# Optimization experiments

Hardware: AMD Instinct MI355X
Metric: run time of the kernel (lower is better)

The kernel has to match this reference:

```python
import jax, jax.numpy as jnp
import numpy as np


def setup_inputs() -> dict:
    key = jax.random.key(0)
    k1, k2 = jax.random.split(key)
    B, T, D, E = 4, 4096, 2048, 64
    x = jax.random.normal(k1, (B, T, D), dtype=jnp.float32)
    # nn.Linear default init ~ U(-1/sqrt(D), 1/sqrt(D)); scaled normal is fine for a numeric baseline
    W = jax.random.normal(k2, (D, E), dtype=jnp.float32) * (1.0 / np.sqrt(D))
    b = jnp.zeros((E,), dtype=jnp.float32)
    return {"x": x, "W": W, "b": b}


TOPK = 2


def reference(x, W, b):
    # logits: (B, T, E)
    logits = jnp.einsum("btd,de->bte", x, W) + b
    probs = jax.nn.softmax(logits, axis=-1)
    topk_vals, topk_idx = jax.lax.top_k(probs, TOPK)
    return topk_idx, topk_vals
```

## Files before the change

### kernel.cpp

```cpp
#include <hip/hip_runtime.h>
#include <math.h>


#define D_DIM 2048
#define E_DIM 64
#define M_DIM 16384
#define RM 32
#define BKC 64
#define NCHW 8
#define XSTR 68

typedef _Float16 half8 __attribute__((ext_vector_type(8)));
typedef float floatx4 __attribute__((ext_vector_type(4)));
typedef unsigned int uint;

__global__ __launch_bounds__(256) void split_w_kernel(
    const float* __restrict__ Wm, _Float16* __restrict__ wsT)
{
    const int tid = threadIdx.x;
    const int n   = tid & 63;
    const int kk0 = tid >> 6;
    const int g   = blockIdx.x;
    #pragma unroll
    for (int r = 0; r < 8; r++) {
        const int kk = kk0 + r * 4;
        const float v = Wm[(size_t)(g * 32 + kk) * E_DIM + n];
        const _Float16 h = (_Float16)v;
        const _Float16 l = (_Float16)((v - (float)h) * 2048.0f);
        const int t = n >> 4, cc = n & 15, qd = kk >> 3, j = kk & 7;
        const size_t base = (size_t)((g * 4 + t) * 2) * 512 + (size_t)(qd * 16 + cc) * 8 + j;
        wsT[base]       = h;
        wsT[base + 512] = l;
    }
}

__global__ __launch_bounds__(256, 2) void router_mfma_kernel(
    const float* __restrict__ x, const _Float16* __restrict__ wsT,
    const float* __restrict__ bias, float* __restrict__ out)
{
    __shared__ uint xbuf[4][2][RM * XSTR];

    const int lane = threadIdx.x & 63;
    const int wave = threadIdx.x >> 6;
    const int c    = lane & 15;
    const int quad = lane >> 4;
    const int c8   = lane & 7;
    const int rq   = lane >> 3;
    const int r0   = blockIdx.x * RM;
    const int kb   = wave * (D_DIM / 4);

    const float* xg = x + (size_t)(r0 + rq) * D_DIM + kb + c8 * 8;
    const _Float16* wbase = wsT + (size_t)(wave * 16) * 4096 + lane * 8;

    floatx4 accm[2][4] = {};
    floatx4 accl[2][4] = {};
    float4 xa[8], xb[8];
    half8 wh0[4], wl0[4], wh1[4], wl1[4];

    auto loadx = [&](int n, float4* dst) {
        const int nn = n < NCHW ? n : NCHW - 1;
        #pragma unroll
        for (int i = 0; i < 4; i++) {
            const float* p = xg + (size_t)i * 8 * D_DIM + nn * BKC;
            dst[2 * i]     = *reinterpret_cast<const float4*>(p);
            dst[2 * i + 1] = *reinterpret_cast<const float4*>(p + 4);
        }
    };
    auto stage = [&](int buf, const float4* src) {
        uint* dst = &xbuf[wave][buf][0];
        #pragma unroll
        for (int i = 0; i < 4; i++) {
            const int row = i * 8 + rq;
            const float f[8] = {src[2 * i].x,     src[2 * i].y,     src[2 * i].z,     src[2 * i].w,
                                src[2 * i + 1].x, src[2 * i + 1].y, src[2 * i + 1].z, src[2 * i + 1].w};
            uint hq[4], lq[4];
            #pragma unroll
            for (int p = 0; p < 4; p++) {
                const float f0 = f[2 * p], f1 = f[2 * p + 1];
                const float h0 = __uint_as_float(__float_as_uint(f0) & 0xFFFFE000u);
                const float h1 = __uint_as_float(__float_as_uint(f1) & 0xFFFFE000u);
                const float l0 = (f0 - h0) * 2048.0f;
                const float l1 = (f1 - h1) * 2048.0f;
                hq[p] = __builtin_bit_cast(uint, __builtin_amdgcn_cvt_pkrtz(h0, h1));
                lq[p] = __builtin_bit_cast(uint, __builtin_amdgcn_cvt_pkrtz(l0, l1));
            }
            *reinterpret_cast<uint4*>(dst + row * XSTR + c8 * 4) =
                make_uint4(hq[0], hq[1], hq[2], hq[3]);
            *reinterpret_cast<uint4*>(dst + row * XSTR + 32 + c8 * 4) =
                make_uint4(lq[0], lq[1], lq[2], lq[3]);
        }
    };
    auto loadW = [&](int u, half8* wh, half8* wl) {
        const int uu = u < 16 ? u : 15;
        const _Float16* p = wbase + (size_t)uu * 4096;
        #pragma unroll
        for (int t = 0; t < 4; t++) {
            wh[t] = *reinterpret_cast<const half8*>(p + t * 1024);
            wl[t] = *reinterpret_cast<const half8*>(p + t * 1024 + 512);
        }
    };
    auto step = [&](int buf, int s, const half8* wh, const half8* wl) {
        #pragma unroll
        for (int tau = 0; tau < 2; tau++) {
            const uint* rp = &xbuf[wave][buf][(tau * 16 + c) * XSTR + s * 16 + quad * 4];
            const uint4 hu = *reinterpret_cast<const uint4*>(rp);
            const uint4 lu = *reinterpret_cast<const uint4*>(rp + 32);
            const half8 ah = __builtin_bit_cast(half8, hu);
            const half8 al = __builtin_bit_cast(half8, lu);
            #pragma unroll
            for (int t = 0; t < 4; t++) {
                accm[tau][t] = __builtin_amdgcn_mfma_f32_16x16x32_f16(ah, wh[t], accm[tau][t], 0, 0, 0);
                accl[tau][t] = __builtin_amdgcn_mfma_f32_16x16x32_f16(al, wh[t], accl[tau][t], 0, 0, 0);
                accl[tau][t] = __builtin_amdgcn_mfma_f32_16x16x32_f16(ah, wl[t], accl[tau][t], 0, 0, 0);
            }
        }
    };

    loadx(0, xa);
    loadx(1, xb);
    loadW(0, wh0, wl0);
    stage(0, xa);

    #pragma unroll 1
    for (int n = 0; n < NCHW; n += 2) {
        loadx(n + 2, xa);
        loadW(2 * n + 1, wh1, wl1);
        stage(1, xb);
        step(0, 0, wh0, wl0);
        loadW(2 * n + 2, wh0, wl0);
        step(0, 1, wh1, wl1);
        loadx(n + 3, xb);
        loadW(2 * n + 3, wh1, wl1);
        if (n + 2 < NCHW) stage(0, xa);
        step(1, 0, wh0, wl0);
        loadW(2 * n + 4, wh0, wl0);
        step(1, 1, wh1, wl1);
    }

    __syncthreads();
    float* red = reinterpret_cast<float*>(&xbuf[0][0][0]);
    const float scale = 1.0f / 2048.0f;
    #pragma unroll
    for (int tau = 0; tau < 2; tau++)
        #pragma unroll
        for (int t = 0; t < 4; t++)
            #pragma unroll
            for (int i = 0; i < 4; i++)
                red[(wave * 32 + tau * 16 + quad * 4 + i) * 65 + c + 16 * t] =
                    accm[tau][t][i] + accl[tau][t][i] * scale;
    __syncthreads();

    if (wave >= 2) return;

    float bvt[4];
    #pragma unroll
    for (int t = 0; t < 4; t++) bvt[t] = bias[c + 16 * t];

    #pragma unroll
    for (int i = 0; i < 4; i++) {
        const int row = wave * 16 + quad * 4 + i;
        float lt[4];
        #pragma unroll
        for (int t = 0; t < 4; t++) {
            const int col = c + 16 * t;
            lt[t] = red[(0 * 32 + row) * 65 + col] + red[(1 * 32 + row) * 65 + col]
                  + red[(2 * 32 + row) * 65 + col] + red[(3 * 32 + row) * 65 + col] + bvt[t];
        }
        const float l0 = lt[0], l1 = lt[1], l2 = lt[2], l3 = lt[3];

        float m = fmaxf(fmaxf(l0, l1), fmaxf(l2, l3));
        #pragma unroll
        for (int off = 1; off < 16; off <<= 1)
            m = fmaxf(m, __shfl_xor(m, off, 64));

        const float e0 = expf(l0 - m), e1 = expf(l1 - m);
        const float e2 = expf(l2 - m), e3 = expf(l3 - m);
        float s = e0 + e1 + e2 + e3;
        #pragma unroll
        for (int off = 1; off < 16; off <<= 1)
            s += __shfl_xor(s, off, 64);

        const float p0 = e0 / s, p1 = e1 / s, p2 = e2 / s, p3 = e3 / s;

        const unsigned long long ka =
            ((unsigned long long)__float_as_uint(p0) << 32) | (unsigned long long)(63 - c);
        const unsigned long long kb_ =
            ((unsigned long long)__float_as_uint(p1) << 32) | (unsigned long long)(47 - c);
        const unsigned long long kc_ =
            ((unsigned long long)__float_as_uint(p2) << 32) | (unsigned long long)(31 - c);
        const unsigned long long kd =
            ((unsigned long long)__float_as_uint(p3) << 32) | (unsigned long long)(15 - c);

        unsigned long long hi1 = ka > kb_ ? ka : kb_, lo1 = ka > kb_ ? kb_ : ka;
        unsigned long long hi2 = kc_ > kd ? kc_ : kd, lo2 = kc_ > kd ? kd : kc_;
        unsigned long long k1 = hi1 > hi2 ? hi1 : hi2;
        unsigned long long mn = hi1 > hi2 ? hi2 : hi1;
        unsigned long long mx = lo1 > lo2 ? lo1 : lo2;
        unsigned long long k2 = mn > mx ? mn : mx;

        #pragma unroll
        for (int off = 1; off < 16; off <<= 1) {
            const unsigned long long o1 = __shfl_xor(k1, off, 64);
            const unsigned long long o2 = __shfl_xor(k2, off, 64);
            const unsigned long long n1 = k1 > o1 ? k1 : o1;
            const unsigned long long w1 = k1 > o1 ? o1 : k1;
            const unsigned long long w2 = k2 > o2 ? k2 : o2;
            k1 = n1;
            k2 = w1 > w2 ? w1 : w2;
        }

        if (c == 0) {
            const int gr = r0 + row;
            out[gr * 2 + 0] = (float)(63 - (int)(k1 & 0xFFFFFFFFull));
            out[gr * 2 + 1] = (float)(63 - (int)(k2 & 0xFFFFFFFFull));
            out[M_DIM * 2 + gr * 2 + 0] = __uint_as_float((unsigned)(k1 >> 32));
            out[M_DIM * 2 + gr * 2 + 1] = __uint_as_float((unsigned)(k2 >> 32));
        }
    }
}

extern "C" void kernel_launch(void* const* d_in, const int* in_sizes, int n_in,
                              void* d_out, int out_size, void* d_ws, size_t ws_size,
                              hipStream_t stream) {
    const float* x  = (const float*)d_in[0];
    const float* Wm = (const float*)d_in[1];
    const float* b  = (const float*)d_in[2];
    float* out = (float*)d_out;
    _Float16* wsT = (_Float16*)d_ws;

    split_w_kernel<<<dim3(64), dim3(256), 0, stream>>>(Wm, wsT);
    router_mfma_kernel<<<dim3(M_DIM / RM), dim3(256), 0, stream>>>(x, wsT, b, out);
}
```

Before: 203.8 us.

## Load x directly into MFMA fragments, removing LDS staging of x

Each lane now loads its x rows straight from global memory in MFMA operand layout and splits them into fp16 hi/lo in registers, with W as the A operand and x as the B operand. This removes the shared-memory round trip for x (stores, reads, bank traffic) and shrinks LDS use to the final reduction buffer, which may allow higher occupancy. The trade-off is less coalesced global loads, since each lane reads 32-byte pieces from 16 different rows per fragment. The output is written transposed to match the swapped operand layout.

```diff
diff --git a/kernel.cpp b/kernel.cpp
--- a/kernel.cpp
+++ b/kernel.cpp
@@ -6,9 +6,6 @@
 #define E_DIM 64
 #define M_DIM 16384
 #define RM 32
-#define BKC 64
-#define NCHW 8
-#define XSTR 68
 
 typedef _Float16 half8 __attribute__((ext_vector_type(8)));
 typedef float floatx4 __attribute__((ext_vector_type(4)));
@@ -38,57 +35,39 @@
     const float* __restrict__ x, const _Float16* __restrict__ wsT,
     const float* __restrict__ bias, float* __restrict__ out)
 {
-    __shared__ uint xbuf[4][2][RM * XSTR];
+    __shared__ float red[4 * RM * 65];
 
     const int lane = threadIdx.x & 63;
     const int wave = threadIdx.x >> 6;
     const int c    = lane & 15;
     const int quad = lane >> 4;
-    const int c8   = lane & 7;
-    const int rq   = lane >> 3;
     const int r0   = blockIdx.x * RM;
     const int kb   = wave * (D_DIM / 4);
 
-    const float* xg = x + (size_t)(r0 + rq) * D_DIM + kb + c8 * 8;
-    const _Float16* wbase = wsT + (size_t)(wave * 16) * 4096 + lane * 8;
+    const float* xg0 = x + (size_t)(r0 + c) * D_DIM + kb + quad * 8;
+    const float* xg1 = xg0 + (size_t)16 * D_DIM;
+    const _Float16* wbase = wsT + (size_t)(wave * 16) * 4096 + (size_t)lane * 8;
 
     floatx4 accm[2][4] = {};
     floatx4 accl[2][4] = {};
-    float4 xa[8], xb[8];
+
+    float4 a0A, a1A, b0A, b1A;
+    float4 a0B, a1B, b0B, b1B;
     half8 wh0[4], wl0[4], wh1[4], wl1[4];
 
-    auto loadx = [&](int n, float4* dst) {
-        const int nn = n < NCHW ? n : NCHW - 1;
-        #pragma unroll
-        for (int i = 0; i < 4; i++) {
-            const float* p = xg + (size_t)i * 8 * D_DIM + nn * BKC;
-            dst[2 * i]     = *reinterpret_cast<const float4*>(p);
-            dst[2 * i + 1] = *reinterpret_cast<const float4*>(p + 4);
-        }
-    };
-    auto stage = [&](int buf, const float4* src) {
-        uint* dst = &xbuf[wave][buf][0];
-        #pragma unroll
-        for (int i = 0; i < 4; i++) {
-            const int row = i * 8 + rq;
-            const float f[8] = {src[2 * i].x,     src[2 * i].y,     src[2 * i].z,     src[2 * i].w,
-                                src[2 * i + 1].x, src[2 * i + 1].y, src[2 * i + 1].z, src[2 * i + 1].w};
-            uint hq[4], lq[4];
-            #pragma unroll
-            for (int p = 0; p < 4; p++) {
-                const float f0 = f[2 * p], f1 = f[2 * p + 1];
-                const float h0 = __uint_as_float(__float_as_uint(f0) & 0xFFFFE000u);
-                const float h1 = __uint_as_float(__float_as_uint(f1) & 0xFFFFE000u);
-                const float l0 = (f0 - h0) * 2048.0f;
-                const float l1 = (f1 - h1) * 2048.0f;
-                hq[p] = __builtin_bit_cast(uint, __builtin_amdgcn_cvt_pkrtz(h0, h1));
-                lq[p] = __builtin_bit_cast(uint, __builtin_amdgcn_cvt_pkrtz(l0, l1));
-            }
-            *reinterpret_cast<uint4*>(dst + row * XSTR + c8 * 4) =
-                make_uint4(hq[0], hq[1], hq[2], hq[3]);
-            *reinterpret_cast<uint4*>(dst + row * XSTR + 32 + c8 * 4) =
-                make_uint4(lq[0], lq[1], lq[2], lq[3]);
-        }
+    auto loadxA = [&](int u) {
+        const int uu = u < 16 ? u : 15;
+        a0A = *reinterpret_cast<const float4*>(xg0 + uu * 32);
+        a1A = *reinterpret_cast<const float4*>(xg0 + uu * 32 + 4);
+        b0A = *reinterpret_cast<const float4*>(xg1 + uu * 32);
+        b1A = *reinterpret_cast<const float4*>(xg1 + uu * 32 + 4);
+    };
+    auto loadxB = [&](int u) {
+        const int uu = u < 16 ? u : 15;
+        a0B = *reinterpret_cast<const float4*>(xg0 + uu * 32);
+        a1B = *reinterpret_cast<const float4*>(xg0 + uu * 32 + 4);
+        b0B = *reinterpret_cast<const float4*>(xg1 + uu * 32);
+        b1B = *reinterpret_cast<const float4*>(xg1 + uu * 32 + 4);
     };
     auto loadW = [&](int u, half8* wh, half8* wl) {
         const int uu = u < 16 ? u : 15;
@@ -99,55 +78,73 @@
             wl[t] = *reinterpret_cast<const half8*>(p + t * 1024 + 512);
         }
     };
-    auto step = [&](int buf, int s, const half8* wh, const half8* wl) {
-        #pragma unroll
-        for (int tau = 0; tau < 2; tau++) {
-            const uint* rp = &xbuf[wave][buf][(tau * 16 + c) * XSTR + s * 16 + quad * 4];
-            const uint4 hu = *reinterpret_cast<const uint4*>(rp);
-            const uint4 lu = *reinterpret_cast<const uint4*>(rp + 32);
-            const half8 ah = __builtin_bit_cast(half8, hu);
-            const half8 al = __builtin_bit_cast(half8, lu);
-            #pragma unroll
-            for (int t = 0; t < 4; t++) {
-                accm[tau][t] = __builtin_amdgcn_mfma_f32_16x16x32_f16(ah, wh[t], accm[tau][t], 0, 0, 0);
-                accl[tau][t] = __builtin_amdgcn_mfma_f32_16x16x32_f16(al, wh[t], accl[tau][t], 0, 0, 0);
-                accl[tau][t] = __builtin_amdgcn_mfma_f32_16x16x32_f16(ah, wl[t], accl[tau][t], 0, 0, 0);
-            }
-        }
-    };
-
-    loadx(0, xa);
-    loadx(1, xb);
+    auto mkfrag = [&](const float4& u0, const float4& u1, half8& h8, half8& l8) {
+        const float f[8] = {u0.x, u0.y, u0.z, u0.w, u1.x, u1.y, u1.z, u1.w};
+        uint hq[4], lq[4];
+        #pragma unroll
+        for (int p = 0; p < 4; p++) {
+            const float f0 = f[2 * p], f1 = f[2 * p + 1];
+            const float h0 = __uint_as_float(__float_as_uint(f0) & 0xFFFFE000u);
+            const float h1 = __uint_as_float(__float_as_uint(f1) & 0xFFFFE000u);
+            hq[p] = __builtin_bit_cast(uint, __builtin_amdgcn_cvt_pkrtz(h0, h1));
+            lq[p] = __builtin_bit_cast(uint,
+                        __builtin_amdgcn_cvt_pkrtz((f0 - h0) * 2048.0f, (f1 - h1) * 2048.0f));
+        }
+        h8 = __builtin_bit_cast(half8, make_uint4(hq[0], hq[1], hq[2], hq[3]));
+        l8 = __builtin_bit_cast(half8, make_uint4(lq[0], lq[1], lq[2], lq[3]));
+    };
+    auto stepA = [&](const half8* wh, const half8* wl) {
+        half8 xh0, xl0, xh1, xl1;
+        mkfrag(a0A, a1A, xh0, xl0);
+        mkfrag(b0A, b1A, xh1, xl1);
+        #pragma unroll
+        for (int t = 0; t < 4; t++) {
+            accm[0][t] = __builtin_amdgcn_mfma_f32_16x16x32_f16(wh[t], xh0, accm[0][t], 0, 0, 0);
+            accl[0][t] = __builtin_amdgcn_mfma_f32_16x16x32_f16(wh[t], xl0, accl[0][t], 0, 0, 0);
+            accl[0][t] = __builtin_amdgcn_mfma_f32_16x16x32_f16(wl[t], xh0, accl[0][t], 0, 0, 0);
+            accm[1][t] = __builtin_amdgcn_mfma_f32_16x16x32_f16(wh[t], xh1, accm[1][t], 0, 0, 0);
+            accl[1][t] = __builtin_amdgcn_mfma_f32_16x16x32_f16(wh[t], xl1, accl[1][t], 0, 0, 0);
+            accl[1][t] = __builtin_amdgcn_mfma_f32_16x16x32_f16(wl[t], xh1, accl[1][t], 0, 0, 0);
+        }
+    };
+    auto stepB = [&](const half8* wh, const half8* wl) {
+        half8 xh0, xl0, xh1, xl1;
+        mkfrag(a0B, a1B, xh0, xl0);
+        mkfrag(b0B, b1B, xh1, xl1);
+        #pragma unroll
+        for (int t = 0; t < 4; t++) {
+            accm[0][t] = __builtin_amdgcn_mfma_f32_16x16x32_f16(wh[t], xh0, accm[0][t], 0, 0, 0);
+            accl[0][t] = __builtin_amdgcn_mfma_f32_16x16x32_f16(wh[t], xl0, accl[0][t], 0, 0, 0);
+            accl[0][t] = __builtin_amdgcn_mfma_f32_16x16x32_f16(wl[t], xh0, accl[0][t], 0, 0, 0);
+            accm[1][t] = __builtin_amdgcn_mfma_f32_16x16x32_f16(wh[t], xh1, accm[1][t], 0, 0, 0);
+            accl[1][t] = __builtin_amdgcn_mfma_f32_16x16x32_f16(wh[t], xl1, accl[1][t], 0, 0, 0);
+            accl[1][t] = __builtin_amdgcn_mfma_f32_16x16x32_f16(wl[t], xh1, accl[1][t], 0, 0, 0);
+        }
+    };
+
+    loadxA(0);
+    loadxB(1);
     loadW(0, wh0, wl0);
-    stage(0, xa);
 
     #pragma unroll 1
-    for (int n = 0; n < NCHW; n += 2) {
-        loadx(n + 2, xa);
-        loadW(2 * n + 1, wh1, wl1);
-        stage(1, xb);
-        step(0, 0, wh0, wl0);
-        loadW(2 * n + 2, wh0, wl0);
-        step(0, 1, wh1, wl1);
-        loadx(n + 3, xb);
-        loadW(2 * n + 3, wh1, wl1);
-        if (n + 2 < NCHW) stage(0, xa);
-        step(1, 0, wh0, wl0);
-        loadW(2 * n + 4, wh0, wl0);
-        step(1, 1, wh1, wl1);
+    for (int u = 0; u < 16; u += 2) {
+        loadW(u + 1, wh1, wl1);
+        stepA(wh0, wl0);
+        loadxA(u + 2);
+        loadW(u + 2, wh0, wl0);
+        stepB(wh1, wl1);
+        loadxB(u + 3);
     }
 
-    __syncthreads();
-    float* red = reinterpret_cast<float*>(&xbuf[0][0][0]);
     const float scale = 1.0f / 2048.0f;
     #pragma unroll
-    for (int tau = 0; tau < 2; tau++)
+    for (int rg = 0; rg < 2; rg++)
         #pragma unroll
         for (int t = 0; t < 4; t++)
             #pragma unroll
             for (int i = 0; i < 4; i++)
-                red[(wave * 32 + tau * 16 + quad * 4 + i) * 65 + c + 16 * t] =
-                    accm[tau][t][i] + accl[tau][t][i] * scale;
+                red[(wave * 32 + rg * 16 + c) * 65 + t * 16 + quad * 4 + i] =
+                    accm[rg][t][i] + accl[rg][t][i] * scale;
     __syncthreads();
 
     if (wave >= 2) return;
```

Result: slower. 219.0 us (+7.4%).
